# Performance work log

Measured on AMD Instinct MI355X. Metric: run time of the kernel, lower is better.

The kernel has to match this reference:

```python
import jax, jax.numpy as jnp
import numpy as np


def _log_kernel(ks, sigma):
    ax = np.arange(-(ks // 2), ks // 2 + 1, dtype=np.float64)
    xx, yy = np.meshgrid(ax, ax, indexing='ij')
    r2 = xx ** 2 + yy ** 2
    gaussian = np.exp(-r2 / (2 * sigma ** 2))
    laplacian = -1.0 / (np.pi * sigma ** 4) * (1.0 - r2 / (2 * sigma ** 2))
    k = laplacian * gaussian
    k = k / np.sum(np.abs(k))
    return jnp.asarray(k, jnp.float32)


def _hpf_kernel(ks):
    if ks == 3:
        k = np.array([[-1, -1, -1], [-1, 8, -1], [-1, -1, -1]], dtype=np.float32)
    else:  # 5
        k = -np.ones((5, 5), dtype=np.float32)
        k[2, 2] = 24.0
    return jnp.asarray(k)


def _lpf_kernel():
    k = np.array([[1, 2, 1], [2, 4, 2], [1, 2, 1]], dtype=np.float32) / 16.0
    return jnp.asarray(k)


def _gabor_kernel(angle, frequency=0.1, sigma_x=2.0, sigma_y=2.0):
    theta = np.radians(angle)
    x, y = np.meshgrid(np.linspace(-3, 3, 7), np.linspace(-3, 3, 7))
    x_t = x * np.cos(theta) + y * np.sin(theta)
    y_t = -x * np.sin(theta) + y * np.cos(theta)
    g = np.exp(-(x_t ** 2 / sigma_x ** 2 + y_t ** 2 / sigma_y ** 2) / 2.0) * np.cos(2 * np.pi * frequency * x_t)
    g = g / np.sum(np.abs(g))
    return jnp.asarray(g, jnp.float32)


def _dwconv(x, k2d, pad):
    # depthwise conv: same single-channel kernel applied to every channel
    C = x.shape[1]
    kern = jnp.broadcast_to(k2d[None, None], (C, 1) + k2d.shape)  # (C,1,kh,kw)
    return jax.lax.conv_general_dilated(
        x, kern, window_strides=(1, 1), padding=[(pad, pad), (pad, pad)],
        feature_group_count=C, dimension_numbers=('NCHW', 'OIHW', 'NCHW'))


def _squash(z):
    # (tanh(z*0.1)+1)/2
    return (jnp.tanh(z * 0.1) + 1.0) * 0.5


def setup_inputs() -> dict:
    key = jax.random.key(0)
    x = jax.random.normal(key, (16, 3, 512, 512), dtype=jnp.float32)
    return {"x": x, "use_gabor": 1}


def reference(x, use_gabor):
    # 'original'
    original = x
    # 'lpf'
    lpf = _dwconv(x, _lpf_kernel(), pad=1)
    # 'log': multi-scale LoG -> squash -> elementwise max over scales
    log3 = _dwconv(x, _log_kernel(3, 0.8), pad=1)
    log5 = _dwconv(x, _log_kernel(5, 1.0), pad=2)
    log7 = _dwconv(x, _log_kernel(7, 1.4), pad=3)
    log_out = jnp.maximum(jnp.maximum(_squash(log3), _squash(log5)), _squash(log7))
    # 'hpf'
    hpf3 = _dwconv(x, _hpf_kernel(3), pad=1)
    hpf5 = _dwconv(x, _hpf_kernel(5), pad=2)
    hpf_out = jnp.maximum(_squash(hpf3), _squash(hpf5))
    outs = (original, lpf, log_out, hpf_out)
    if use_gabor:
        gab = None
        for angle in (0, 45, 90, 135):
            r = jnp.tanh(_dwconv(x, _gabor_kernel(angle), pad=3) * 0.1)
            gab = r if gab is None else jnp.maximum(gab, r)
        outs = outs + (gab,)
    return outs
```

## Files before the change

kernel.cpp:

```cpp
#include <hip/hip_runtime.h>

#define IMG_H 512
#define IMG_W 512
#define TILE_W 64
#define TILE_H 16
#define LDSW 72
#define LDSH 22
#define TCOLS 72
#define TROWS 16
#define NTHREADS 256


constexpr double PI_D = 3.141592653589793238462643383279502884;

constexpr double cexp(double x) {
  double term = 1.0, sum = 1.0;
  for (int n = 1; n < 48; ++n) { term *= x / n; sum += term; }
  return sum;
}
constexpr double ccos(double x) {
  double term = 1.0, sum = 1.0;
  for (int n = 1; n < 24; ++n) {
    term *= -x * x / ((2.0 * n - 1.0) * (2.0 * n));
    sum += term;
  }
  return sum;
}
constexpr double csin(double x) {
  double term = x, sum = x;
  for (int n = 1; n < 24; ++n) {
    term *= -x * x / ((2.0 * n) * (2.0 * n + 1.0));
    sum += term;
  }
  return sum;
}
constexpr double cabs_(double x) { return x < 0 ? -x : x; }

constexpr void fill_log(int ks, double sigma, float* out) {
  double buf[49] = {};
  double s = 0.0;
  const int h = ks / 2;
  for (int i = 0; i < ks; ++i) {
    for (int j = 0; j < ks; ++j) {
      const double xi = (double)(i - h);
      const double yj = (double)(j - h);
      const double r2 = xi * xi + yj * yj;
      const double g = cexp(-r2 / (2.0 * sigma * sigma));
      const double lap = -1.0 / (PI_D * sigma * sigma * sigma * sigma) *
                         (1.0 - r2 / (2.0 * sigma * sigma));
      buf[i * ks + j] = lap * g;
      s += cabs_(lap * g);
    }
  }
  for (int k = 0; k < ks * ks; ++k) out[k] = (float)(buf[k] / s);
}

constexpr void fill_log_sep(int ks, double sigma, float* va, float* g, float* wb) {
  const int h = ks / 2;
  double s = 0.0;
  for (int i = 0; i < ks; ++i)
    for (int j = 0; j < ks; ++j) {
      const double xi = (double)(i - h), yj = (double)(j - h);
      const double r2 = xi * xi + yj * yj;
      const double gg = cexp(-r2 / (2.0 * sigma * sigma));
      const double lap = -1.0 / (PI_D * sigma * sigma * sigma * sigma) *
                         (1.0 - r2 / (2.0 * sigma * sigma));
      s += cabs_(lap * gg);
    }
  const double c = 1.0 / (PI_D * sigma * sigma * sigma * sigma);
  for (int i = 0; i < ks; ++i) {
    const double d = (double)(i - h);
    const double gi = cexp(-d * d / (2.0 * sigma * sigma));
    g[i] = (float)gi;
    va[i] = (float)((-c + c * d * d / (2.0 * sigma * sigma)) * gi / s);
    wb[i] = (float)((c * d * d / (2.0 * sigma * sigma)) * gi / s);
  }
}

constexpr double gabor_norm(double ang_deg) {
  const double th = ang_deg * PI_D / 180.0;
  const double ct = ccos(th), st = csin(th);
  double s = 0.0;
  for (int i = 0; i < 7; ++i)
    for (int j = 0; j < 7; ++j) {
      const double xv = (double)(j - 3);
      const double yv = (double)(i - 3);
      const double xt = xv * ct + yv * st;
      const double yt = -xv * st + yv * ct;
      const double g = cexp(-(xt * xt / 4.0 + yt * yt / 4.0) / 2.0) *
                       ccos(2.0 * PI_D * 0.1 * xt);
      s += cabs_(g);
    }
  return s;
}

struct SepTabs {
  float l5_va[5], l5_g[5], l5_wb[5];
  float l7_va[7], l7_g[7], l7_wb[7];
  float v_gb[7], v_gc0[7], v_gca[7], v_gsa[7];
  float h_g0[7], h_g90[7], h_gc[7], h_gs[7];
  float is45, is135;
  float l3_m, l3_e, l3_s;
};

constexpr SepTabs make_sep() {
  SepTabs t{};
  fill_log_sep(5, 1.0, t.l5_va, t.l5_g, t.l5_wb);
  fill_log_sep(7, 1.4, t.l7_va, t.l7_g, t.l7_wb);
  const double s0 = gabor_norm(0.0), s90 = gabor_norm(90.0);
  const double s45 = gabor_norm(45.0), s135 = gabor_norm(135.0);
  const double th45 = 45.0 * PI_D / 180.0;
  const double a45 = 2.0 * PI_D * 0.1 * ccos(th45);
  const double b45 = 2.0 * PI_D * 0.1 * csin(th45);
  const double w0 = 2.0 * PI_D * 0.1;
  for (int k = 0; k < 7; ++k) {
    const double d = (double)(k - 3);
    const double gg = cexp(-d * d / 8.0);
    t.v_gb[k]  = (float)gg;
    t.v_gc0[k] = (float)(gg * ccos(w0 * d));
    t.v_gca[k] = (float)(gg * ccos(b45 * d));
    t.v_gsa[k] = (float)(gg * csin(b45 * d));
    t.h_g0[k]  = (float)(gg * ccos(w0 * d) / s0);
    t.h_g90[k] = (float)(gg / s90);
    t.h_gc[k]  = (float)(gg * ccos(a45 * d));
    t.h_gs[k]  = (float)(gg * csin(a45 * d));
  }
  t.is45 = (float)(1.0 / s45);
  t.is135 = (float)(1.0 / s135);
  float l3[9] = {};
  fill_log(3, 0.8, l3);
  t.l3_m = l3[4]; t.l3_e = l3[1]; t.l3_s = l3[0];
  return t;
}

constexpr SepTabs ST = make_sep();


__device__ __forceinline__ float fast_tanh(float x) {
  float e = __builtin_amdgcn_exp2f(x * 2.8853900817779268f);
  return 1.0f - 2.0f * __builtin_amdgcn_rcpf(e + 1.0f);
}
__device__ __forceinline__ float squash_from(float z) {
  return fmaf(fast_tanh(0.1f * z), 0.5f, 0.5f);
}
__device__ __forceinline__ float4 f4z() { return make_float4(0.f, 0.f, 0.f, 0.f); }
__device__ __forceinline__ float4 f4add(float4 a, float4 b) {
  return make_float4(a.x + b.x, a.y + b.y, a.z + b.z, a.w + b.w);
}
__device__ __forceinline__ float4 f4fma(float a, float4 b, float4 c) {
  return make_float4(fmaf(a, b.x, c.x), fmaf(a, b.y, c.y),
                     fmaf(a, b.z, c.z), fmaf(a, b.w, c.w));
}
__device__ __forceinline__ void loadw12(const float* p, float* w) {
  const float4 a = *(const float4*)(p);
  const float4 b = *(const float4*)(p + 4);
  const float4 c = *(const float4*)(p + 8);
  w[0] = a.x; w[1] = a.y; w[2] = a.z; w[3] = a.w;
  w[4] = b.x; w[5] = b.y; w[6] = b.z; w[7] = b.w;
  w[8] = c.x; w[9] = c.y; w[10] = c.z; w[11] = c.w;
}

#define T_B5  0
#define T_L5A 1
#define T_L5G 2
#define T_L7A 3
#define T_L7G 4
#define T_GB  5
#define T_GC0 6
#define T_GCA 7
#define T_GSA 8

__global__ __launch_bounds__(NTHREADS)
void msif_kernel(const float* __restrict__ x, float* __restrict__ out,
                 int planes, int do_gab) {
  __shared__ float tile[LDSH * LDSW];
  __shared__ float T[9][TROWS * TCOLS];

  const int tid = threadIdx.x;
  const int tx = tid & 15;
  const int ty = tid >> 4;
  const int x0 = blockIdx.x * TILE_W;
  const int y0 = blockIdx.y * TILE_H;
  const int plane = blockIdx.z;
  const float* __restrict__ in = x + (size_t)plane * (IMG_H * IMG_W);

  const int gx0 = x0 - 4;
  const int gy0 = y0 - 3;
  for (int k = tid; k < LDSH * (LDSW / 4); k += NTHREADS) {
    int r = k / (LDSW / 4);
    int cc = (k - r * (LDSW / 4)) * 4;
    int gy = gy0 + r;
    int gx = gx0 + cc;
    float4 v = make_float4(0.f, 0.f, 0.f, 0.f);
    if ((unsigned)gy < IMG_H) {
      const float* rowp = in + (size_t)gy * IMG_W;
      if (gx >= 0 && gx + 3 < IMG_W) {
        v = *(const float4*)(rowp + gx);
      } else {
        float t0 = 0.f, t1 = 0.f, t2 = 0.f, t3 = 0.f;
        if ((unsigned)(gx + 0) < IMG_W) t0 = rowp[gx + 0];
        if ((unsigned)(gx + 1) < IMG_W) t1 = rowp[gx + 1];
        if ((unsigned)(gx + 2) < IMG_W) t2 = rowp[gx + 2];
        if ((unsigned)(gx + 3) < IMG_W) t3 = rowp[gx + 3];
        v = make_float4(t0, t1, t2, t3);
      }
    }
    *(float4*)&tile[r * LDSW + cc] = v;
  }
  __syncthreads();

  for (int k = tid; k < TROWS * (TCOLS / 4); k += NTHREADS) {
    const int r = k / (TCOLS / 4);
    const int c4 = (k - r * (TCOLS / 4)) * 4;
    const float* base = &tile[r * LDSW + c4];
    float4 wv[7];
#pragma unroll
    for (int i = 0; i < 7; ++i) wv[i] = *(const float4*)(base + i * LDSW);

    float4 b5 = f4add(f4add(wv[1], wv[2]), f4add(f4add(wv[3], wv[4]), wv[5]));
    float4 l5a = f4z(), l5g = f4z();
#pragma unroll
    for (int i = 0; i < 5; ++i) {
      l5a = f4fma(ST.l5_va[i], wv[i + 1], l5a);
      l5g = f4fma(ST.l5_g[i],  wv[i + 1], l5g);
    }
    float4 l7a = f4z(), l7g = f4z(), gb = f4z(), gc0 = f4z(), gca = f4z(), gsa = f4z();
#pragma unroll
    for (int i = 0; i < 7; ++i) {
      l7a = f4fma(ST.l7_va[i], wv[i], l7a);
      l7g = f4fma(ST.l7_g[i],  wv[i], l7g);
      gb  = f4fma(ST.v_gb[i],  wv[i], gb);
      gc0 = f4fma(ST.v_gc0[i], wv[i], gc0);
      gca = f4fma(ST.v_gca[i], wv[i], gca);
      gsa = f4fma(ST.v_gsa[i], wv[i], gsa);
    }
    const int o = r * TCOLS + c4;
    *(float4*)&T[T_B5][o]  = b5;
    *(float4*)&T[T_L5A][o] = l5a;
    *(float4*)&T[T_L5G][o] = l5g;
    *(float4*)&T[T_L7A][o] = l7a;
    *(float4*)&T[T_L7G][o] = l7g;
    *(float4*)&T[T_GB][o]  = gb;
    *(float4*)&T[T_GC0][o] = gc0;
    *(float4*)&T[T_GCA][o] = gca;
    *(float4*)&T[T_GSA][o] = gsa;
  }
  __syncthreads();

  const int toff = ty * TCOLS + 4 * tx;
  float w[12];
  float l7[4] = {}, l5[4] = {}, g0[4] = {}, g90[4] = {}, Pa[4] = {}, Qa[4] = {};
  float box[4];

  loadw12(&T[T_L7A][toff], w);
#pragma unroll
  for (int dx = 0; dx < 7; ++dx) {
    const float cc = ST.l7_g[dx];
#pragma unroll
    for (int c = 0; c < 4; ++c) l7[c] = fmaf(w[c + dx + 1], cc, l7[c]);
  }
  loadw12(&T[T_L7G][toff], w);
#pragma unroll
  for (int dx = 0; dx < 7; ++dx) {
    const float cc = ST.l7_wb[dx];
#pragma unroll
    for (int c = 0; c < 4; ++c) l7[c] = fmaf(w[c + dx + 1], cc, l7[c]);
  }
  loadw12(&T[T_L5A][toff], w);
#pragma unroll
  for (int dx = 0; dx < 5; ++dx) {
    const float cc = ST.l5_g[dx];
#pragma unroll
    for (int c = 0; c < 4; ++c) l5[c] = fmaf(w[c + dx + 2], cc, l5[c]);
  }
  loadw12(&T[T_L5G][toff], w);
#pragma unroll
  for (int dx = 0; dx < 5; ++dx) {
    const float cc = ST.l5_wb[dx];
#pragma unroll
    for (int c = 0; c < 4; ++c) l5[c] = fmaf(w[c + dx + 2], cc, l5[c]);
  }
  loadw12(&T[T_B5][toff], w);
#pragma unroll
  for (int c = 0; c < 4; ++c)
    box[c] = ((w[c + 2] + w[c + 3]) + (w[c + 4] + w[c + 5])) + w[c + 6];
  loadw12(&T[T_GB][toff], w);
#pragma unroll
  for (int dx = 0; dx < 7; ++dx) {
    const float cc = ST.h_g0[dx];
#pragma unroll
    for (int c = 0; c < 4; ++c) g0[c] = fmaf(w[c + dx + 1], cc, g0[c]);
  }
  loadw12(&T[T_GC0][toff], w);
#pragma unroll
  for (int dx = 0; dx < 7; ++dx) {
    const float cc = ST.h_g90[dx];
#pragma unroll
    for (int c = 0; c < 4; ++c) g90[c] = fmaf(w[c + dx + 1], cc, g90[c]);
  }
  loadw12(&T[T_GCA][toff], w);
#pragma unroll
  for (int dx = 0; dx < 7; ++dx) {
    const float cc = ST.h_gc[dx];
#pragma unroll
    for (int c = 0; c < 4; ++c) Pa[c] = fmaf(w[c + dx + 1], cc, Pa[c]);
  }
  loadw12(&T[T_GSA][toff], w);
#pragma unroll
  for (int dx = 0; dx < 7; ++dx) {
    const float cc = ST.h_gs[dx];
#pragma unroll
    for (int c = 0; c < 4; ++c) Qa[c] = fmaf(w[c + dx + 1], cc, Qa[c]);
  }

  float tr[12], mr[12], br[12];
  loadw12(&tile[(ty + 2) * LDSW + 4 * tx], tr);
  loadw12(&tile[(ty + 3) * LDSW + 4 * tx], mr);
  loadw12(&tile[(ty + 4) * LDSW + 4 * tx], br);

  const int X = x0 + 4 * tx;
  const int yo = y0 + ty;
  const size_t fs = (size_t)planes * (IMG_H * IMG_W);
  const size_t off = (size_t)plane * (IMG_H * IMG_W) + (size_t)yo * IMG_W + X;

  *(float4*)(out + off) = make_float4(mr[4], mr[5], mr[6], mr[7]);

  float lp[4], lo[4], ho[4], go[4];
#pragma unroll
  for (int c = 0; c < 4; ++c) {
    const float mC = mr[c + 4];
    const float e  = (tr[c + 4] + br[c + 4]) + (mr[c + 3] + mr[c + 5]);
    const float sC = (tr[c + 3] + tr[c + 5]) + (br[c + 3] + br[c + 5]);
    lp[c] = fmaf(0.25f, mC, fmaf(0.125f, e, 0.0625f * sC));
    const float l3v = fmaf(ST.l3_m, mC, fmaf(ST.l3_e, e, ST.l3_s * sC));
    const float h3v = fmaf(8.f, mC, -(e + sC));
    const float h5v = fmaf(25.f, mC, -box[c]);
    lo[c] = squash_from(fmaxf(fmaxf(l3v, l5[c]), l7[c]));
    ho[c] = squash_from(fmaxf(h3v, h5v));
    const float o45  = (Pa[c] - Qa[c]) * ST.is45;
    const float o135 = (Pa[c] + Qa[c]) * ST.is135;
    go[c] = fast_tanh(0.1f * fmaxf(fmaxf(g0[c], g90[c]), fmaxf(o45, o135)));
  }
  *(float4*)(out + fs + off) = make_float4(lp[0], lp[1], lp[2], lp[3]);
  *(float4*)(out + 2 * fs + off) = make_float4(lo[0], lo[1], lo[2], lo[3]);
  *(float4*)(out + 3 * fs + off) = make_float4(ho[0], ho[1], ho[2], ho[3]);
  if (do_gab)
    *(float4*)(out + 4 * fs + off) = make_float4(go[0], go[1], go[2], go[3]);
}

extern "C" void kernel_launch(void* const* d_in, const int* in_sizes, int n_in,
                              void* d_out, int out_size, void* d_ws, size_t ws_size,
                              hipStream_t stream) {
  const float* x = (const float*)d_in[0];
  float* out = (float*)d_out;
  const int plane_elems = IMG_H * IMG_W;
  const int planes = in_sizes[0] / plane_elems;
  const int do_gab = (out_size >= 5 * in_sizes[0]) ? 1 : 0;

  dim3 grid(IMG_W / TILE_W, IMG_H / TILE_H, planes);
  msif_kernel<<<grid, NTHREADS, 0, stream>>>(x, out, planes, do_gab);
}
```

Before: 328.5 us.

## Split separable passes into two phases to shrink LDS and raise occupancy

The shared intermediate buffer goes from nine to five planes. The LoG/box vertical passes run and are consumed first, then the Gabor vertical passes reuse the same LDS slots after an extra barrier. Launch bounds now request five blocks per CU, which cuts LDS per block and caps registers, aiming for more resident waves to hide memory latency. In exchange it adds two barriers and a second sweep over the tile, and the register cap risks spills.

New measurement: 312.3 us. 1.05x faster.

```diff
diff --git a/kernel.cpp b/kernel.cpp
--- a/kernel.cpp
+++ b/kernel.cpp
@@ -8,6 +8,7 @@
 #define LDSH 22
 #define TCOLS 72
 #define TROWS 16
+#define NSLOTA (TROWS * (TCOLS / 4))
 #define NTHREADS 256
 
 
@@ -160,21 +161,12 @@
   w[8] = c.x; w[9] = c.y; w[10] = c.z; w[11] = c.w;
 }
 
-#define T_B5  0
-#define T_L5A 1
-#define T_L5G 2
-#define T_L7A 3
-#define T_L7G 4
-#define T_GB  5
-#define T_GC0 6
-#define T_GCA 7
-#define T_GSA 8
-
-__global__ __launch_bounds__(NTHREADS)
+
+__global__ __launch_bounds__(NTHREADS, 5)
 void msif_kernel(const float* __restrict__ x, float* __restrict__ out,
                  int planes, int do_gab) {
   __shared__ float tile[LDSH * LDSW];
-  __shared__ float T[9][TROWS * TCOLS];
+  __shared__ float T[5][TROWS * TCOLS];
 
   const int tid = threadIdx.x;
   const int tx = tid & 15;
@@ -197,19 +189,17 @@
       if (gx >= 0 && gx + 3 < IMG_W) {
         v = *(const float4*)(rowp + gx);
       } else {
-        float t0 = 0.f, t1 = 0.f, t2 = 0.f, t3 = 0.f;
-        if ((unsigned)(gx + 0) < IMG_W) t0 = rowp[gx + 0];
-        if ((unsigned)(gx + 1) < IMG_W) t1 = rowp[gx + 1];
-        if ((unsigned)(gx + 2) < IMG_W) t2 = rowp[gx + 2];
-        if ((unsigned)(gx + 3) < IMG_W) t3 = rowp[gx + 3];
-        v = make_float4(t0, t1, t2, t3);
+        if ((unsigned)(gx + 0) < IMG_W) v.x = rowp[gx + 0];
+        if ((unsigned)(gx + 1) < IMG_W) v.y = rowp[gx + 1];
+        if ((unsigned)(gx + 2) < IMG_W) v.z = rowp[gx + 2];
+        if ((unsigned)(gx + 3) < IMG_W) v.w = rowp[gx + 3];
       }
     }
     *(float4*)&tile[r * LDSW + cc] = v;
   }
   __syncthreads();
 
-  for (int k = tid; k < TROWS * (TCOLS / 4); k += NTHREADS) {
+  for (int k = tid; k < NSLOTA; k += NTHREADS) {
     const int r = k / (TCOLS / 4);
     const int c4 = (k - r * (TCOLS / 4)) * 4;
     const float* base = &tile[r * LDSW + c4];
@@ -224,128 +214,165 @@
       l5a = f4fma(ST.l5_va[i], wv[i + 1], l5a);
       l5g = f4fma(ST.l5_g[i],  wv[i + 1], l5g);
     }
-    float4 l7a = f4z(), l7g = f4z(), gb = f4z(), gc0 = f4z(), gca = f4z(), gsa = f4z();
+    float4 l7a = f4z(), l7g = f4z();
 #pragma unroll
     for (int i = 0; i < 7; ++i) {
       l7a = f4fma(ST.l7_va[i], wv[i], l7a);
       l7g = f4fma(ST.l7_g[i],  wv[i], l7g);
-      gb  = f4fma(ST.v_gb[i],  wv[i], gb);
-      gc0 = f4fma(ST.v_gc0[i], wv[i], gc0);
-      gca = f4fma(ST.v_gca[i], wv[i], gca);
-      gsa = f4fma(ST.v_gsa[i], wv[i], gsa);
     }
     const int o = r * TCOLS + c4;
-    *(float4*)&T[T_B5][o]  = b5;
-    *(float4*)&T[T_L5A][o] = l5a;
-    *(float4*)&T[T_L5G][o] = l5g;
-    *(float4*)&T[T_L7A][o] = l7a;
-    *(float4*)&T[T_L7G][o] = l7g;
-    *(float4*)&T[T_GB][o]  = gb;
-    *(float4*)&T[T_GC0][o] = gc0;
-    *(float4*)&T[T_GCA][o] = gca;
-    *(float4*)&T[T_GSA][o] = gsa;
+    *(float4*)&T[0][o] = b5;
+    *(float4*)&T[1][o] = l5a;
+    *(float4*)&T[2][o] = l5g;
+    *(float4*)&T[3][o] = l7a;
+    *(float4*)&T[4][o] = l7g;
   }
   __syncthreads();
 
+  const size_t fs = (size_t)planes * (IMG_H * IMG_W);
+  const size_t off = (size_t)plane * (IMG_H * IMG_W) +
+                     (size_t)(y0 + ty) * IMG_W + (x0 + 4 * tx);
   const int toff = ty * TCOLS + 4 * tx;
-  float w[12];
-  float l7[4] = {}, l5[4] = {}, g0[4] = {}, g90[4] = {}, Pa[4] = {}, Qa[4] = {};
-  float box[4];
-
-  loadw12(&T[T_L7A][toff], w);
-#pragma unroll
-  for (int dx = 0; dx < 7; ++dx) {
-    const float cc = ST.l7_g[dx];
-#pragma unroll
-    for (int c = 0; c < 4; ++c) l7[c] = fmaf(w[c + dx + 1], cc, l7[c]);
-  }
-  loadw12(&T[T_L7G][toff], w);
-#pragma unroll
-  for (int dx = 0; dx < 7; ++dx) {
-    const float cc = ST.l7_wb[dx];
-#pragma unroll
-    for (int c = 0; c < 4; ++c) l7[c] = fmaf(w[c + dx + 1], cc, l7[c]);
-  }
-  loadw12(&T[T_L5A][toff], w);
-#pragma unroll
-  for (int dx = 0; dx < 5; ++dx) {
-    const float cc = ST.l5_g[dx];
-#pragma unroll
-    for (int c = 0; c < 4; ++c) l5[c] = fmaf(w[c + dx + 2], cc, l5[c]);
-  }
-  loadw12(&T[T_L5G][toff], w);
-#pragma unroll
-  for (int dx = 0; dx < 5; ++dx) {
-    const float cc = ST.l5_wb[dx];
-#pragma unroll
-    for (int c = 0; c < 4; ++c) l5[c] = fmaf(w[c + dx + 2], cc, l5[c]);
-  }
-  loadw12(&T[T_B5][toff], w);
-#pragma unroll
-  for (int c = 0; c < 4; ++c)
-    box[c] = ((w[c + 2] + w[c + 3]) + (w[c + 4] + w[c + 5])) + w[c + 6];
-  loadw12(&T[T_GB][toff], w);
-#pragma unroll
-  for (int dx = 0; dx < 7; ++dx) {
-    const float cc = ST.h_g0[dx];
-#pragma unroll
-    for (int c = 0; c < 4; ++c) g0[c] = fmaf(w[c + dx + 1], cc, g0[c]);
-  }
-  loadw12(&T[T_GC0][toff], w);
-#pragma unroll
-  for (int dx = 0; dx < 7; ++dx) {
-    const float cc = ST.h_g90[dx];
-#pragma unroll
-    for (int c = 0; c < 4; ++c) g90[c] = fmaf(w[c + dx + 1], cc, g90[c]);
-  }
-  loadw12(&T[T_GCA][toff], w);
-#pragma unroll
-  for (int dx = 0; dx < 7; ++dx) {
-    const float cc = ST.h_gc[dx];
-#pragma unroll
-    for (int c = 0; c < 4; ++c) Pa[c] = fmaf(w[c + dx + 1], cc, Pa[c]);
-  }
-  loadw12(&T[T_GSA][toff], w);
-#pragma unroll
-  for (int dx = 0; dx < 7; ++dx) {
-    const float cc = ST.h_gs[dx];
-#pragma unroll
-    for (int c = 0; c < 4; ++c) Qa[c] = fmaf(w[c + dx + 1], cc, Qa[c]);
-  }
-
-  float tr[12], mr[12], br[12];
-  loadw12(&tile[(ty + 2) * LDSW + 4 * tx], tr);
-  loadw12(&tile[(ty + 3) * LDSW + 4 * tx], mr);
-  loadw12(&tile[(ty + 4) * LDSW + 4 * tx], br);
-
-  const int X = x0 + 4 * tx;
-  const int yo = y0 + ty;
-  const size_t fs = (size_t)planes * (IMG_H * IMG_W);
-  const size_t off = (size_t)plane * (IMG_H * IMG_W) + (size_t)yo * IMG_W + X;
-
-  *(float4*)(out + off) = make_float4(mr[4], mr[5], mr[6], mr[7]);
-
-  float lp[4], lo[4], ho[4], go[4];
-#pragma unroll
-  for (int c = 0; c < 4; ++c) {
-    const float mC = mr[c + 4];
-    const float e  = (tr[c + 4] + br[c + 4]) + (mr[c + 3] + mr[c + 5]);
-    const float sC = (tr[c + 3] + tr[c + 5]) + (br[c + 3] + br[c + 5]);
-    lp[c] = fmaf(0.25f, mC, fmaf(0.125f, e, 0.0625f * sC));
-    const float l3v = fmaf(ST.l3_m, mC, fmaf(ST.l3_e, e, ST.l3_s * sC));
-    const float h3v = fmaf(8.f, mC, -(e + sC));
-    const float h5v = fmaf(25.f, mC, -box[c]);
-    lo[c] = squash_from(fmaxf(fmaxf(l3v, l5[c]), l7[c]));
-    ho[c] = squash_from(fmaxf(h3v, h5v));
-    const float o45  = (Pa[c] - Qa[c]) * ST.is45;
-    const float o135 = (Pa[c] + Qa[c]) * ST.is135;
-    go[c] = fast_tanh(0.1f * fmaxf(fmaxf(g0[c], g90[c]), fmaxf(o45, o135)));
-  }
-  *(float4*)(out + fs + off) = make_float4(lp[0], lp[1], lp[2], lp[3]);
-  *(float4*)(out + 2 * fs + off) = make_float4(lo[0], lo[1], lo[2], lo[3]);
-  *(float4*)(out + 3 * fs + off) = make_float4(ho[0], ho[1], ho[2], ho[3]);
-  if (do_gab)
+
+  {
+    float w[12];
+    float l7[4] = {}, l5[4] = {}, box[4];
+
+    loadw12(&T[3][toff], w);
+#pragma unroll
+    for (int dx = 0; dx < 7; ++dx) {
+      const float cc = ST.l7_g[dx];
+#pragma unroll
+      for (int c = 0; c < 4; ++c) l7[c] = fmaf(w[c + dx + 1], cc, l7[c]);
+    }
+    loadw12(&T[4][toff], w);
+#pragma unroll
+    for (int dx = 0; dx < 7; ++dx) {
+      const float cc = ST.l7_wb[dx];
+#pragma unroll
+      for (int c = 0; c < 4; ++c) l7[c] = fmaf(w[c + dx + 1], cc, l7[c]);
+    }
+    loadw12(&T[1][toff], w);
+#pragma unroll
+    for (int dx = 0; dx < 5; ++dx) {
+      const float cc = ST.l5_g[dx];
+#pragma unroll
+      for (int c = 0; c < 4; ++c) l5[c] = fmaf(w[c + dx + 2], cc, l5[c]);
+    }
+    loadw12(&T[2][toff], w);
+#pragma unroll
+    for (int dx = 0; dx < 5; ++dx) {
+      const float cc = ST.l5_wb[dx];
+#pragma unroll
+      for (int c = 0; c < 4; ++c) l5[c] = fmaf(w[c + dx + 2], cc, l5[c]);
+    }
+    loadw12(&T[0][toff], w);
+#pragma unroll
+    for (int c = 0; c < 4; ++c)
+      box[c] = ((w[c + 2] + w[c + 3]) + (w[c + 4] + w[c + 5])) + w[c + 6];
+
+    float m[4], e[4], s[4];
+    loadw12(&tile[(ty + 2) * LDSW + 4 * tx], w);
+#pragma unroll
+    for (int c = 0; c < 4; ++c) {
+      e[c] = w[c + 4];
+      s[c] = w[c + 3] + w[c + 5];
+    }
+    loadw12(&tile[(ty + 4) * LDSW + 4 * tx], w);
+#pragma unroll
+    for (int c = 0; c < 4; ++c) {
+      e[c] += w[c + 4];
+      s[c] += w[c + 3] + w[c + 5];
+    }
+    loadw12(&tile[(ty + 3) * LDSW + 4 * tx], w);
+    *(float4*)(out + off) = make_float4(w[4], w[5], w[6], w[7]);
+#pragma unroll
+    for (int c = 0; c < 4; ++c) {
+      m[c] = w[c + 4];
+      e[c] += w[c + 3] + w[c + 5];
+    }
+
+    float lp[4], lo[4], ho[4];
+#pragma unroll
+    for (int c = 0; c < 4; ++c) {
+      lp[c] = fmaf(0.25f, m[c], fmaf(0.125f, e[c], 0.0625f * s[c]));
+      const float l3v = fmaf(ST.l3_m, m[c], fmaf(ST.l3_e, e[c], ST.l3_s * s[c]));
+      const float h3v = fmaf(8.f, m[c], -(e[c] + s[c]));
+      const float h5v = fmaf(25.f, m[c], -box[c]);
+      lo[c] = squash_from(fmaxf(fmaxf(l3v, l5[c]), l7[c]));
+      ho[c] = squash_from(fmaxf(h3v, h5v));
+    }
+    *(float4*)(out + fs + off) = make_float4(lp[0], lp[1], lp[2], lp[3]);
+    *(float4*)(out + 2 * fs + off) = make_float4(lo[0], lo[1], lo[2], lo[3]);
+    *(float4*)(out + 3 * fs + off) = make_float4(ho[0], ho[1], ho[2], ho[3]);
+  }
+
+  if (!do_gab) return;
+  __syncthreads();
+
+  for (int k = tid; k < NSLOTA; k += NTHREADS) {
+    const int r = k / (TCOLS / 4);
+    const int c4 = (k - r * (TCOLS / 4)) * 4;
+    const float* base = &tile[r * LDSW + c4];
+    float4 gb = f4z(), gc0 = f4z(), gca = f4z(), gsa = f4z();
+#pragma unroll
+    for (int i = 0; i < 7; ++i) {
+      const float4 wv = *(const float4*)(base + i * LDSW);
+      gb  = f4fma(ST.v_gb[i],  wv, gb);
+      gc0 = f4fma(ST.v_gc0[i], wv, gc0);
+      gca = f4fma(ST.v_gca[i], wv, gca);
+      gsa = f4fma(ST.v_gsa[i], wv, gsa);
+    }
+    const int o = r * TCOLS + c4;
+    *(float4*)&T[0][o] = gb;
+    *(float4*)&T[1][o] = gc0;
+    *(float4*)&T[2][o] = gca;
+    *(float4*)&T[3][o] = gsa;
+  }
+  __syncthreads();
+
+  {
+    float w[12];
+    float g0[4] = {}, g90[4] = {}, Pa[4] = {}, Qa[4] = {};
+
+    loadw12(&T[0][toff], w);
+#pragma unroll
+    for (int dx = 0; dx < 7; ++dx) {
+      const float cc = ST.h_g0[dx];
+#pragma unroll
+      for (int c = 0; c < 4; ++c) g0[c] = fmaf(w[c + dx + 1], cc, g0[c]);
+    }
+    loadw12(&T[1][toff], w);
+#pragma unroll
+    for (int dx = 0; dx < 7; ++dx) {
+      const float cc = ST.h_g90[dx];
+#pragma unroll
+      for (int c = 0; c < 4; ++c) g90[c] = fmaf(w[c + dx + 1], cc, g90[c]);
+    }
+    loadw12(&T[2][toff], w);
+#pragma unroll
+    for (int dx = 0; dx < 7; ++dx) {
+      const float cc = ST.h_gc[dx];
+#pragma unroll
+      for (int c = 0; c < 4; ++c) Pa[c] = fmaf(w[c + dx + 1], cc, Pa[c]);
+    }
+    loadw12(&T[3][toff], w);
+#pragma unroll
+    for (int dx = 0; dx < 7; ++dx) {
+      const float cc = ST.h_gs[dx];
+#pragma unroll
+      for (int c = 0; c < 4; ++c) Qa[c] = fmaf(w[c + dx + 1], cc, Qa[c]);
+    }
+
+    float go[4];
+#pragma unroll
+    for (int c = 0; c < 4; ++c) {
+      const float o45  = (Pa[c] - Qa[c]) * ST.is45;
+      const float o135 = (Pa[c] + Qa[c]) * ST.is135;
+      go[c] = fast_tanh(0.1f * fmaxf(fmaxf(g0[c], g90[c]), fmaxf(o45, o135)));
+    }
     *(float4*)(out + 4 * fs + off) = make_float4(go[0], go[1], go[2], go[3]);
+  }
 }
 
 extern "C" void kernel_launch(void* const* d_in, const int* in_sizes, int n_in,
```
